# Kernel optimization log

Hardware: AMD Instinct MI355X
Metric: run time of the kernel (lower is better)

Reference implementation:

```python
import jax, jax.numpy as jnp
import numpy as np

P = 16                     # patch size
D = 192                    # embed dim (forced by SAT d_model=192)
NHEAD = 3                  # ViT-Tiny heads
SAT_H, SAT_DK, SAT_DV = 8, 32, 32
N_SLICE = 10
PER_LI = jnp.linspace(0.1, 1.0, N_SLICE)
LN_EPS = 1e-5


def layernorm(z, g, b):
    m = z.mean(-1, keepdims=True)
    v = ((z - m) ** 2).mean(-1, keepdims=True)
    return (z - m) * jax.lax.rsqrt(v + LN_EPS) * g + b


def setup_inputs() -> dict:
    key = jax.random.key(0)
    ks = jax.random.split(key, 32)
    B, IMG, DEPTH, MLP = 128, 224, 12, 4 * D
    S = (IMG // P) ** 2 + 1  # 197 tokens
    n = lambda k, sh: jax.random.normal(k, sh, jnp.float32) * 0.02
    z = lambda sh: jnp.zeros(sh, jnp.float32)
    o = lambda sh: jnp.ones(sh, jnp.float32)
    return {
        "x": jax.random.uniform(ks[0], (B, 3, IMG, IMG), jnp.float32),
        "x_g_norm": jax.random.uniform(ks[1], (B, 1, 56, 56), jnp.float32),
        "patch_w": n(ks[2], (D, 3, P, P)), "patch_b": z((D,)),
        "cls_token": n(ks[3], (1, 1, D)), "pos_embed": n(ks[4], (1, S, D)),
        "eleva_embed": n(ks[5], (1, D)),
        "sat_wq": n(ks[6], (D, SAT_H * SAT_DK)), "sat_bq": z((SAT_H * SAT_DK,)),
        "sat_wk": n(ks[7], (D, SAT_H * SAT_DK)), "sat_bk": z((SAT_H * SAT_DK,)),
        "sat_wv": n(ks[8], (D, SAT_H * SAT_DV)), "sat_bv": z((SAT_H * SAT_DV,)),
        "sat_wo": n(ks[9], (SAT_H * SAT_DV, D)), "sat_bo": z((D,)),
        "ln1_g": o((DEPTH, D)), "ln1_b": z((DEPTH, D)),
        "qkv_w": n(ks[10], (DEPTH, D, 3 * D)), "qkv_b": z((DEPTH, 3 * D)),
        "proj_w": n(ks[11], (DEPTH, D, D)), "proj_b": z((DEPTH, D)),
        "ln2_g": o((DEPTH, D)), "ln2_b": z((DEPTH, D)),
        "fc1_w": n(ks[12], (DEPTH, D, MLP)), "fc1_b": z((DEPTH, MLP)),
        "fc2_w": n(ks[13], (DEPTH, MLP, D)), "fc2_b": z((DEPTH, D)),
        "norm_g": o((D,)), "norm_b": z((D,)),
    }


def _forward(x, x_g_norm, patch_w, patch_b, cls_token, pos_embed, eleva_embed,
             sat_wq, sat_bq, sat_wk, sat_bk, sat_wv, sat_bv, sat_wo, sat_bo,
             ln1_g, ln1_b, qkv_w, qkv_b, proj_w, proj_b, ln2_g, ln2_b,
             fc1_w, fc1_b, fc2_w, fc2_b, norm_g, norm_b):
    B = x.shape[0]
    # --- patch embed: Conv2d(3, D, kernel=P, stride=P) -> [B, N, D] ---
    feat = jax.lax.conv_general_dilated(
        x, patch_w, (P, P), 'VALID', dimension_numbers=('NCHW', 'OIHW', 'NCHW'))
    feat = feat + patch_b[None, :, None, None]
    tokens = feat.reshape(B, D, -1).transpose(0, 2, 1)          # [B, 196, D]
    tok = jnp.concatenate([jnp.broadcast_to(cls_token, (B, 1, D)), tokens], axis=1)
    tok = tok + pos_embed                                        # [B, S, D]
    S = tok.shape[1]
    # --- elevation weight per sample (vectorized bisect + linear interp) ---
    means = x_g_norm.mean(axis=(1, 2, 3))                        # [B]
    idx = jnp.clip(jnp.searchsorted(PER_LI, means, side='left'), 0, N_SLICE - 1)
    per_hi = PER_LI[idx]
    per_lo = jnp.where(idx == 0, 0.0, PER_LI[jnp.maximum(idx - 1, 0)])
    idx_f = idx.astype(jnp.float32)
    idx_inter = idx_f - (per_hi - means) / (per_hi - per_lo)
    w = jnp.where(idx == N_SLICE - 1, idx_f, idx_inter) / N_SLICE  # [B]
    # --- SAT fusion: per (batch, token) a 2-element attention over (token, ele) ---
    ele = jnp.broadcast_to(eleva_embed[0] * w[:, None, None], tok.shape)  # [B,S,D]
    at_in = jnp.stack([tok, ele], axis=2)                        # [B, S, 2, D]
    q = (at_in @ sat_wq + sat_bq).reshape(B, S, 2, SAT_H, SAT_DK)
    k = (at_in @ sat_wk + sat_bk).reshape(B, S, 2, SAT_H, SAT_DK)
    v = (at_in @ sat_wv + sat_bv).reshape(B, S, 2, SAT_H, SAT_DV)
    att = jnp.einsum('bsqhd,bskhd->bshqk', q, k) * (1.0 / np.sqrt(SAT_DK))
    att = jax.nn.softmax(att, axis=-1)
    sat_o = jnp.einsum('bshqk,bskhd->bsqhd', att, v).reshape(B, S, 2, SAT_H * SAT_DV)
    sat_o = sat_o @ sat_wo + sat_bo                              # [B, S, 2, D]
    h = sat_o[..., 0, :] + sat_o[..., 1, :]                      # [B, S, D]
    # --- ViT blocks via scan over stacked layer params ---
    hd = D // NHEAD

    def block(z, p):
        l1g, l1b, qw, qb, pw, pb, l2g, l2b, f1w, f1b, f2w, f2b = p
        y = layernorm(z, l1g, l1b)
        qkv = y @ qw + qb                                        # [B, S, 3D]
        q_, k_, v_ = jnp.split(qkv, 3, axis=-1)
        q_ = q_.reshape(B, S, NHEAD, hd)
        k_ = k_.reshape(B, S, NHEAD, hd)
        v_ = v_.reshape(B, S, NHEAD, hd)
        a = jnp.einsum('bqhd,bkhd->bhqk', q_, k_) * (hd ** -0.5)
        a = jax.nn.softmax(a, axis=-1)
        o = jnp.einsum('bhqk,bkhd->bqhd', a, v_).reshape(B, S, D)
        z = z + o @ pw + pb
        y = layernorm(z, l2g, l2b)
        z = z + jax.nn.gelu(y @ f1w + f1b, approximate=False) @ f2w + f2b
        return z, None

    h, _ = jax.lax.scan(block, h, (ln1_g, ln1_b, qkv_w, qkv_b, proj_w, proj_b,
                                   ln2_g, ln2_b, fc1_w, fc1_b, fc2_w, fc2_b))
    h = layernorm(h, norm_g, norm_b)
    return h[:, 0]                                               # [B, D] cls token


def reference(x, x_g_norm, patch_w, patch_b, cls_token, pos_embed, eleva_embed,
              sat_wq, sat_bq, sat_wk, sat_bk, sat_wv, sat_bv, sat_wo, sat_bo,
              ln1_g, ln1_b, qkv_w, qkv_b, proj_w, proj_b, ln2_g, ln2_b,
              fc1_w, fc1_b, fc2_w, fc2_b, norm_g, norm_b):
    return _forward(x, x_g_norm, patch_w, patch_b, cls_token, pos_embed, eleva_embed,
                    sat_wq, sat_bq, sat_wk, sat_bk, sat_wv, sat_bv, sat_wo, sat_bo,
                    ln1_g, ln1_b, qkv_w, qkv_b, proj_w, proj_b, ln2_g, ln2_b,
                    fc1_w, fc1_b, fc2_w, fc2_b, norm_g, norm_b)
```

## Files before the change

kernel.cpp:

```cpp
#include <hip/hip_runtime.h>


#define BATCH 128
#define SEQ 197
#define BS_ROWS (BATCH * SEQ)
#define DMODEL 192
#define NPATCH 196
#define MROWS_PATCH (BATCH * NPATCH)
#define KPATCH 768
#define MLPDIM 768
#define DEPTH 12
#define SPAD 224

typedef float f32x4 __attribute__((ext_vector_type(4)));
typedef short s16x8 __attribute__((ext_vector_type(8)));

__device__ __forceinline__ float wredSum(float v) {
#pragma unroll
  for (int o = 32; o > 0; o >>= 1) v += __shfl_xor(v, o, 64);
  return v;
}

__device__ __forceinline__ unsigned short f2bf(float f) {
  union { float f; unsigned u; } v;
  v.f = f;
  unsigned r = v.u + 0x7FFFu + ((v.u >> 16) & 1u);
  return (unsigned short)(r >> 16);
}
__device__ __forceinline__ float bf2f(unsigned short u) {
  union { unsigned u; float f; } v;
  v.u = ((unsigned)u) << 16;
  return v.f;
}

__device__ __forceinline__ int swz(int col, int row) {
  int g8 = col >> 3;
  g8 = (g8 & ~7) | ((g8 & 7) ^ (row & 7));
  return (g8 << 3) | (col & 7);
}

__device__ __forceinline__ float gelu(float x) {
  const float ax = fabsf(x) * 0.70710678118654752f;
  const float t = 1.f / (1.f + 0.3275911f * ax);
  const float y =
      t * (0.254829592f +
           t * (-0.284496736f +
                t * (1.421413741f + t * (-1.453152027f + t * 1.061405429f))));
  const float erfc_ = y * __expf(-ax * ax);
  const float cdf = (x >= 0.f) ? (1.f - 0.5f * erfc_) : (0.5f * erfc_);
  return x * cdf;
}

__global__ __launch_bounds__(256) void eleva_w_kernel(const float* __restrict__ xg,
                                                      float* __restrict__ wout) {
  const int b = blockIdx.x;
  const float* p = xg + (size_t)b * 3136;
  float s = 0.f;
  for (int i = threadIdx.x; i < 3136; i += 256) s += p[i];
  __shared__ float partial[4];
  s = wredSum(s);
  if ((threadIdx.x & 63) == 0) partial[threadIdx.x >> 6] = s;
  __syncthreads();
  if (threadIdx.x == 0) {
    float m = (partial[0] + partial[1] + partial[2] + partial[3]) / 3136.f;
    int idx = 0;
#pragma unroll
    for (int i = 0; i < 10; i++) {
      float pv = 0.1f * (float)(i + 1);
      if (pv < m) idx = i + 1;
    }
    if (idx > 9) idx = 9;
    float wv;
    if (idx == 9) {
      wv = 9.f;
    } else {
      float hi = 0.1f * (float)(idx + 1);
      float lo = (idx == 0) ? 0.f : 0.1f * (float)idx;
      wv = (float)idx - (hi - m) / (hi - lo);
    }
    wout[b] = wv / 10.f;
  }
}

__global__ __launch_bounds__(256) void wtrans_kernel(const float* __restrict__ in,
                                                     unsigned short* __restrict__ out,
                                                     int R, int C) {
  const int z = blockIdx.z;
  in += (size_t)z * R * C;
  out += (size_t)z * R * C;
  const int c0 = blockIdx.x * 32, r0 = blockIdx.y * 32;
  __shared__ float t[32][33];
  const int tr = threadIdx.x >> 3, tc = (threadIdx.x & 7) * 4;
  const float4 v = *(const float4*)(in + (size_t)(r0 + tr) * C + c0 + tc);
  t[tr][tc] = v.x; t[tr][tc + 1] = v.y; t[tr][tc + 2] = v.z; t[tr][tc + 3] = v.w;
  __syncthreads();
  ushort4 o;
  o.x = f2bf(t[tc + 0][tr]);
  o.y = f2bf(t[tc + 1][tr]);
  o.z = f2bf(t[tc + 2][tr]);
  o.w = f2bf(t[tc + 3][tr]);
  const int brow = c0 + tr;
  *(ushort4*)(out + (size_t)brow * R + swz(r0 + tc, brow)) = o;
}

__global__ __launch_bounds__(256) void convert_kernel(const float* __restrict__ in,
                                                      unsigned short* __restrict__ out, int n4,
                                                      int K) {
  const int i = blockIdx.x * 256 + threadIdx.x;
  if (i >= n4) return;
  const int flat = i * 4;
  const int row = flat / K, col = flat % K;
  const float4 v = *(const float4*)(in + flat);
  ushort4 o;
  o.x = f2bf(v.x); o.y = f2bf(v.y); o.z = f2bf(v.z); o.w = f2bf(v.w);
  *(ushort4*)(out + (size_t)row * K + swz(col, row)) = o;
}

__global__ __launch_bounds__(256) void im2col_kernel(const float* __restrict__ x,
                                                     unsigned short* __restrict__ col) {
  const int i = blockIdx.x * 256 + threadIdx.x;
  if (i >= MROWS_PATCH * KPATCH / 8) return;
  const int k = (i % 96) * 8, row = i / 96;
  const int b = row / NPATCH, p = row % NPATCH;
  const int py = p / 14, px = p % 14;
  const int c = k >> 8, r = (k >> 4) & 15, cc = k & 15;
  const float* src = x + (((size_t)b * 3 + c) * 224 + (py * 16 + r)) * 224 + (px * 16 + cc);
  const float4 v0 = *(const float4*)src;
  const float4 v1 = *(const float4*)(src + 4);
  s16x8 o;
  o[0] = (short)f2bf(v0.x); o[1] = (short)f2bf(v0.y);
  o[2] = (short)f2bf(v0.z); o[3] = (short)f2bf(v0.w);
  o[4] = (short)f2bf(v1.x); o[5] = (short)f2bf(v1.y);
  o[6] = (short)f2bf(v1.z); o[7] = (short)f2bf(v1.w);
  *(s16x8*)(col + (size_t)row * KPATCH + swz(k, row)) = o;
}

__global__ __launch_bounds__(256) void cls_kernel(const float* __restrict__ cls,
                                                  const float* __restrict__ pos,
                                                  float* __restrict__ H,
                                                  unsigned short* __restrict__ Hbf) {
  const int i = blockIdx.x * 256 + threadIdx.x;
  if (i >= BATCH * DMODEL) return;
  const int b = i / DMODEL, d = i % DMODEL;
  const float v = cls[d] + pos[d];
  const int row = b * SEQ;
  H[(size_t)row * DMODEL + d] = v;
  Hbf[(size_t)row * DMODEL + swz(d, row)] = f2bf(v);
}

__global__ __launch_bounds__(256) void ele_proj_kernel(
    const float* __restrict__ ele_emb, const float* __restrict__ wq, const float* __restrict__ bq,
    const float* __restrict__ wk, const float* __restrict__ bk,
    const float* __restrict__ wv, const float* __restrict__ bv,
    const float* __restrict__ wvec, float* __restrict__ eq, float* __restrict__ ek,
    float* __restrict__ ev, float* __restrict__ satb) {
  const int b = blockIdx.x, t = threadIdx.x;
  if (b == 0) {
    satb[t] = bq[t];
    satb[256 + t] = bk[t];
    satb[512 + t] = bv[t];
  }
  __shared__ float es[DMODEL];
  if (t < DMODEL) es[t] = ele_emb[t] * wvec[b];
  __syncthreads();
  float aq = bq[t], ak = bk[t], av = bv[t];
  for (int d = 0; d < DMODEL; d++) {
    const float e = es[d];
    aq += e * wq[d * 256 + t];
    ak += e * wk[d * 256 + t];
    av += e * wv[d * 256 + t];
  }
  eq[b * 256 + t] = aq;
  ek[b * 256 + t] = ak;
  ev[b * 256 + t] = av;
}

__global__ __launch_bounds__(256) void sat_mix_kernel(
    const unsigned short* __restrict__ qkv768, const float* __restrict__ eq,
    const float* __restrict__ ek, const float* __restrict__ ev,
    unsigned short* __restrict__ o256) {
  const int gid = blockIdx.x * 256 + threadIdx.x;
  const int tok = gid >> 3, h = gid & 7;
  if (tok >= BS_ROWS) return;
  const int b = tok / SEQ;
  const unsigned short* qp = qkv768 + (size_t)tok * 768 + h * 32;
  s16x8 qv[4], kv[4];
#pragma unroll
  for (int i0 = 0; i0 < 4; i0++) {
    qv[i0] = *(const s16x8*)(qp + i0 * 8);
    kv[i0] = *(const s16x8*)(qp + 256 + i0 * 8);
  }
  float eqa[32], eka[32];
  {
    const float4* eqp = (const float4*)(eq + b * 256 + h * 32);
    const float4* ekp = (const float4*)(ek + b * 256 + h * 32);
#pragma unroll
    for (int i0 = 0; i0 < 8; i0++) {
      const float4 a = eqp[i0], c = ekp[i0];
      eqa[i0 * 4] = a.x; eqa[i0 * 4 + 1] = a.y; eqa[i0 * 4 + 2] = a.z; eqa[i0 * 4 + 3] = a.w;
      eka[i0 * 4] = c.x; eka[i0 * 4 + 1] = c.y; eka[i0 * 4 + 2] = c.z; eka[i0 * 4 + 3] = c.w;
    }
  }
  float s00 = 0.f, s01 = 0.f, s10 = 0.f, s11 = 0.f;
#pragma unroll
  for (int d = 0; d < 32; d++) {
    const float q_ = bf2f((unsigned short)qv[d >> 3][d & 7]);
    const float k_ = bf2f((unsigned short)kv[d >> 3][d & 7]);
    s00 += q_ * k_;
    s01 += q_ * eka[d];
    s10 += eqa[d] * k_;
    s11 += eqa[d] * eka[d];
  }
  const float sc = 0.17677669529663687f;
  s00 *= sc; s01 *= sc; s10 *= sc; s11 *= sc;
  const float m0 = fmaxf(s00, s01), m1 = fmaxf(s10, s11);
  const float e00 = __expf(s00 - m0), e01 = __expf(s01 - m0);
  const float e10 = __expf(s10 - m1), e11 = __expf(s11 - m1);
  const float w0 = e00 / (e00 + e01) + e10 / (e10 + e11);
  const float w1 = e01 / (e00 + e01) + e11 / (e10 + e11);
  unsigned short* op = o256 + (size_t)tok * 256;
  const float4* evp = (const float4*)(ev + b * 256 + h * 32);
#pragma unroll
  for (int i0 = 0; i0 < 4; i0++) {
    const s16x8 vv = *(const s16x8*)(qp + 512 + i0 * 8);
    const float4 e0 = evp[i0 * 2], e1 = evp[i0 * 2 + 1];
    float ev8[8] = {e0.x, e0.y, e0.z, e0.w, e1.x, e1.y, e1.z, e1.w};
    s16x8 o;
#pragma unroll
    for (int e = 0; e < 8; e++)
      o[e] = (short)f2bf(w0 * bf2f((unsigned short)vv[e]) + w1 * ev8[e]);
    *(s16x8*)(op + swz(h * 32 + i0 * 8, tok)) = o;
  }
}

template <int EPI, bool SWZO, int BN, int BM>
__global__ __launch_bounds__(256, 4)
void gemm_mfma(const unsigned short* __restrict__ A,
               const unsigned short* __restrict__ Bt,
               const float* __restrict__ bias,
               const float* __restrict__ res,
               void* __restrict__ Cout,
               unsigned short* __restrict__ aux_hbf,
               const float* __restrict__ aux_pos,
               const float* __restrict__ lng,
               const float* __restrict__ lnb,
               int M, int N, int K) {
  constexpr int NJ = 3;
  constexpr int MI = (BM == 128) ? 4 : 2;
  constexpr bool LNF = (EPI == 5 || EPI == 6);
  constexpr int LNROWS = LNF ? BM : 1;
  __shared__ unsigned short As[BM * 64];
  __shared__ unsigned short Bs[BN * 64];
  __shared__ float2 lnbuf[4][LNROWS];
  const int tid = threadIdx.x, lane = tid & 63, w = tid >> 6;
  const int n0 = blockIdx.x * BN;
  const int m0 = blockIdx.y * BM;
  const int c = lane & 15, g = lane >> 4;
  const int wm = (BM == 128) ? (w >> 1) * 64 : 0;
  const int wn = (BM == 128) ? (w & 1) * 96 / 2 : w * 48;
  f32x4 acc[MI][NJ] = {};

  const int ar = (lane >> 3);
  const int acol = (lane & 7) * 8;

  for (int k0 = 0; k0 < K; k0 += 64) {
#pragma unroll
    for (int it = 0; it < BM / 32; it++) {
      const int r = w * (BM / 4) + it * 8 + ar;
      const unsigned short* gp = A + (size_t)(m0 + r) * K + k0 + acol;
      __builtin_amdgcn_global_load_lds(
          (const __attribute__((address_space(1))) unsigned int*)gp,
          (__attribute__((address_space(3))) unsigned int*)(As + (w * (BM / 4) + it * 8) * 64),
          16, 0, 0);
    }
#pragma unroll
    for (int it = 0; it < BN / 32; it++) {
      const int r = w * (BN / 4) + it * 8 + ar;
      const unsigned short* gp = Bt + (size_t)(n0 + r) * K + k0 + acol;
      __builtin_amdgcn_global_load_lds(
          (const __attribute__((address_space(1))) unsigned int*)gp,
          (__attribute__((address_space(3))) unsigned int*)(Bs + (w * (BN / 4) + it * 8) * 64),
          16, 0, 0);
    }
    __syncthreads();
#pragma unroll
    for (int kk = 0; kk < 2; kk++) {
      const int sw = (((kk * 4 + g) ^ (c & 7))) << 3;
      s16x8 af[MI], bfr[NJ];
#pragma unroll
      for (int i = 0; i < MI; i++)
        af[i] = *(const s16x8*)&As[(wm + i * 16 + c) * 64 + sw];
#pragma unroll
      for (int j = 0; j < NJ; j++)
        bfr[j] = *(const s16x8*)&Bs[(wn + j * 16 + c) * 64 + sw];
#pragma unroll
      for (int i = 0; i < MI; i++)
#pragma unroll
        for (int j = 0; j < NJ; j++)
          acc[i][j] = __builtin_amdgcn_mfma_f32_16x16x32_bf16(af[i], bfr[j], acc[i][j], 0, 0, 0);
    }
    __syncthreads();
  }

  const int ncol0 = n0 + wn + c;
  float bv[NJ];
#pragma unroll
  for (int j = 0; j < NJ; j++) bv[j] = bias[ncol0 + j * 16] * (EPI == 6 ? 2.f : 1.f);

  if constexpr (LNF) {
#pragma unroll
    for (int i = 0; i < MI; i++) {
#pragma unroll
      for (int r_ = 0; r_ < 4; r_++) {
        const int lr = wm + i * 16 + g * 4 + r_;
        const int mrow = m0 + lr;
        float s1 = 0.f, s2 = 0.f;
#pragma unroll
        for (int j = 0; j < NJ; j++) {
          float v = acc[i][j][r_] + bv[j];
          if (EPI == 5) v += res[(size_t)mrow * DMODEL + ncol0 + j * 16];
          acc[i][j][r_] = v;
          ((float*)Cout)[(size_t)mrow * DMODEL + ncol0 + j * 16] = v;
          s1 += v;
          s2 += v * v;
        }
#pragma unroll
        for (int o = 1; o <= 8; o <<= 1) {
          s1 += __shfl_xor(s1, o, 64);
          s2 += __shfl_xor(s2, o, 64);
        }
        if (c == 0) lnbuf[w][lr] = make_float2(s1, s2);
      }
    }
    __syncthreads();
    float lg[NJ], lb[NJ];
#pragma unroll
    for (int j = 0; j < NJ; j++) { lg[j] = lng[ncol0 + j * 16]; lb[j] = lnb[ncol0 + j * 16]; }
#pragma unroll
    for (int i = 0; i < MI; i++) {
#pragma unroll
      for (int r_ = 0; r_ < 4; r_++) {
        const int lr = wm + i * 16 + g * 4 + r_;
        const int mrow = m0 + lr;
        const float2 a0 = lnbuf[0][lr], a1 = lnbuf[1][lr];
        const float2 a2 = lnbuf[2][lr], a3 = lnbuf[3][lr];
        const float mean = (a0.x + a1.x + a2.x + a3.x) * (1.f / 192.f);
        const float var = (a0.y + a1.y + a2.y + a3.y) * (1.f / 192.f) - mean * mean;
        const float inv = rsqrtf(var + 1e-5f);
#pragma unroll
        for (int j = 0; j < NJ; j++) {
          const int col = ncol0 + j * 16;
          const float yn = (acc[i][j][r_] - mean) * inv * lg[j] + lb[j];
          aux_hbf[(size_t)mrow * DMODEL + swz(col, mrow)] = f2bf(yn);
        }
      }
    }
  } else {
#pragma unroll
    for (int i = 0; i < MI; i++) {
#pragma unroll
      for (int r_ = 0; r_ < 4; r_++) {
        const int mrow = m0 + wm + i * 16 + g * 4 + r_;
        if (EPI == 4) {
          const int bb = mrow / 196;
          const int p = mrow - bb * 196;
          const int drow = mrow + bb + 1;
#pragma unroll
          for (int j = 0; j < NJ; j++) {
            const int col = ncol0 + j * 16;
            const float v = acc[i][j][r_] + bv[j] + aux_pos[(size_t)(p + 1) * DMODEL + col];
            ((float*)Cout)[(size_t)drow * DMODEL + col] = v;
            aux_hbf[(size_t)drow * DMODEL + swz(col, drow)] = f2bf(v);
          }
        } else {
#pragma unroll
          for (int j = 0; j < NJ; j++) {
            float v = acc[i][j][r_] + bv[j];
            const int col = ncol0 + j * 16;
            const size_t rowoff = (size_t)mrow * N;
            if (EPI == 0) {
              ((unsigned short*)Cout)[rowoff + (SWZO ? swz(col, mrow) : col)] = f2bf(v);
            } else {
              ((unsigned short*)Cout)[rowoff + (SWZO ? swz(col, mrow) : col)] = f2bf(gelu(v));
            }
          }
        }
      }
    }
  }
}

__global__ __launch_bounds__(256) void final_ln_kernel(const float* __restrict__ H,
                                                       const float* __restrict__ g,
                                                       const float* __restrict__ bta,
                                                       float* __restrict__ out) {
  const int w = threadIdx.x >> 6, lane = threadIdx.x & 63;
  const int bi = blockIdx.x * 4 + w;
  if (bi >= BATCH) return;
  const float* x = H + (size_t)bi * SEQ * DMODEL;
  const float x0 = x[lane], x1 = x[lane + 64], x2 = x[lane + 128];
  const float m = wredSum(x0 + x1 + x2) * (1.f / 192.f);
  const float d0 = x0 - m, d1 = x1 - m, d2 = x2 - m;
  const float v = wredSum(d0 * d0 + d1 * d1 + d2 * d2) * (1.f / 192.f);
  const float inv = rsqrtf(v + 1e-5f);
  float* y = out + (size_t)bi * DMODEL;
  y[lane] = d0 * inv * g[lane] + bta[lane];
  y[lane + 64] = d1 * inv * g[lane + 64] + bta[lane + 64];
  y[lane + 128] = d2 * inv * g[lane + 128] + bta[lane + 128];
}

__global__ __launch_bounds__(256) void vtrans_kernel(const unsigned short* __restrict__ qkv,
                                                     unsigned short* __restrict__ vt) {
  const int bid = blockIdx.x;
  const int sc = bid & 3, bh = bid >> 2;
  const int b = bh / 3, h = bh % 3;
  const int s0 = sc * 64;
  __shared__ unsigned short t[64][72];
  const int tid = threadIdx.x;
  for (int e = tid; e < 64 * 64; e += 256) {
    const int sp = e >> 6, d = e & 63;
    const int s = s0 + sp;
    t[sp][d] = (s < SEQ) ? qkv[((size_t)(b * SEQ + s)) * 576 + 384 + h * 64 + d] : (unsigned short)0;
  }
  __syncthreads();
  for (int e = tid; e < 64 * 64; e += 256) {
    const int d = e >> 6, sp = e & 63;
    const int s = s0 + sp;
    if (s < SPAD) vt[((size_t)bh * 64 + d) * SPAD + s] = t[sp][d];
  }
}

__global__ __launch_bounds__(64) void attn_mfma_kernel(const unsigned short* __restrict__ qkv,
                                                       const unsigned short* __restrict__ vt,
                                                       unsigned short* __restrict__ out) {
  const int bid = blockIdx.x;
  const int bh = bid / 13, qt = bid % 13;
  const int b = bh / 3, h = bh % 3;
  const int row0 = b * SEQ;
  const int q0 = qt * 16;
  const int lane = threadIdx.x;
  const int c = lane & 15, g = lane >> 4;

  __shared__ __attribute__((aligned(16))) unsigned short P[16][232];

  const int qr = row0 + min(q0 + c, SEQ - 1);
  const unsigned short* qp = qkv + (size_t)qr * 576 + h * 64 + g * 8;
  const s16x8 qlo = *(const s16x8*)qp;
  const s16x8 qhi = *(const s16x8*)(qp + 32);

  f32x4 acc[13];
#pragma unroll
  for (int t = 0; t < 13; t++) {
    const int kr = row0 + min(t * 16 + c, SEQ - 1);
    const unsigned short* kp = qkv + (size_t)kr * 576 + 192 + h * 64 + g * 8;
    const s16x8 klo = *(const s16x8*)kp;
    const s16x8 khi = *(const s16x8*)(kp + 32);
    f32x4 z = {0.f, 0.f, 0.f, 0.f};
    z = __builtin_amdgcn_mfma_f32_16x16x32_bf16(qlo, klo, z, 0, 0, 0);
    acc[t] = __builtin_amdgcn_mfma_f32_16x16x32_bf16(qhi, khi, z, 0, 0, 0);
  }

  const bool m12 = (c >= 5);
#pragma unroll
  for (int r = 0; r < 4; r++) {
    float mx = -INFINITY;
#pragma unroll
    for (int t = 0; t < 13; t++) {
      const float v = (t == 12 && m12) ? -INFINITY : acc[t][r];
      mx = fmaxf(mx, v);
    }
#pragma unroll
    for (int o = 1; o <= 8; o <<= 1) mx = fmaxf(mx, __shfl_xor(mx, o, 64));
    const float ms = mx * 0.125f;
    float sum = 0.f;
#pragma unroll
    for (int t = 0; t < 13; t++) {
      const float e = (t == 12 && m12) ? 0.f : __expf(acc[t][r] * 0.125f - ms);
      acc[t][r] = e;
      sum += e;
    }
#pragma unroll
    for (int o = 1; o <= 8; o <<= 1) sum += __shfl_xor(sum, o, 64);
    const float inv = 1.f / sum;
#pragma unroll
    for (int t = 0; t < 13; t++) P[g * 4 + r][t * 16 + c] = f2bf(acc[t][r] * inv);
  }
  {
    unsigned short z4[4] = {0, 0, 0, 0};
    *(uint2*)&P[c][208 + g * 4] = *(uint2*)z4;
  }
  __builtin_amdgcn_s_waitcnt(0);

  f32x4 oacc[4];
#pragma unroll
  for (int dt = 0; dt < 4; dt++) oacc[dt] = (f32x4){0.f, 0.f, 0.f, 0.f};
  const unsigned short* vbase = vt + (size_t)bh * 64 * SPAD;
#pragma unroll
  for (int ch = 0; ch < 7; ch++) {
    const s16x8 pa = *(const s16x8*)&P[c][ch * 32 + g * 8];
#pragma unroll
    for (int dt = 0; dt < 4; dt++) {
      const s16x8 vb = *(const s16x8*)(vbase + (size_t)(dt * 16 + c) * SPAD + ch * 32 + g * 8);
      oacc[dt] = __builtin_amdgcn_mfma_f32_16x16x32_bf16(pa, vb, oacc[dt], 0, 0, 0);
    }
  }

#pragma unroll
  for (int dt = 0; dt < 4; dt++) {
#pragma unroll
    for (int r = 0; r < 4; r++) {
      const int q = q0 + g * 4 + r;
      if (q < SEQ) {
        const int trow = row0 + q;
        out[(size_t)trow * DMODEL + swz(h * 64 + dt * 16 + c, trow)] = f2bf(oacc[dt][r]);
      }
    }
  }
}

extern "C" void kernel_launch(void* const* d_in, const int* in_sizes, int n_in,
                              void* d_out, int out_size, void* d_ws, size_t ws_size,
                              hipStream_t stream) {
  const float* x       = (const float*)d_in[0];
  const float* xg      = (const float*)d_in[1];
  const float* patch_w = (const float*)d_in[2];
  const float* patch_b = (const float*)d_in[3];
  const float* cls_tok = (const float*)d_in[4];
  const float* pos_emb = (const float*)d_in[5];
  const float* ele_emb = (const float*)d_in[6];
  const float* sat_wq  = (const float*)d_in[7];
  const float* sat_bq  = (const float*)d_in[8];
  const float* sat_wk  = (const float*)d_in[9];
  const float* sat_bk  = (const float*)d_in[10];
  const float* sat_wv  = (const float*)d_in[11];
  const float* sat_bv  = (const float*)d_in[12];
  const float* sat_wo  = (const float*)d_in[13];
  const float* sat_bo  = (const float*)d_in[14];
  const float* ln1_g   = (const float*)d_in[15];
  const float* ln1_b   = (const float*)d_in[16];
  const float* qkv_w   = (const float*)d_in[17];
  const float* qkv_b   = (const float*)d_in[18];
  const float* proj_w  = (const float*)d_in[19];
  const float* proj_b  = (const float*)d_in[20];
  const float* ln2_g   = (const float*)d_in[21];
  const float* ln2_b   = (const float*)d_in[22];
  const float* fc1_w   = (const float*)d_in[23];
  const float* fc1_b   = (const float*)d_in[24];
  const float* fc2_w   = (const float*)d_in[25];
  const float* fc2_b   = (const float*)d_in[26];
  const float* norm_g  = (const float*)d_in[27];
  const float* norm_b  = (const float*)d_in[28];
  float* out = (float*)d_out;
  float* ws = (float*)d_ws;

  float* W_ELE = ws;
  float* EQ = ws + 256;
  float* EK = EQ + 32768;
  float* EV = EK + 32768;
  float* H = ws + 98560;
  unsigned short* Hbf   = (unsigned short*)(ws + 4940032);
  unsigned short* Ybf   = (unsigned short*)(ws + 7360768);
  unsigned short* QKVbf = (unsigned short*)(ws + 9781504);
  unsigned short* MLPbf = (unsigned short*)(ws + 17043712);
  unsigned short* VTB   = (unsigned short*)(ws + 26726656);
  unsigned short* WTS   = (unsigned short*)(ws + 29479168);
  float* SATB = ws + 32305408;
  unsigned short* ATTNbf = (unsigned short*)(ws + 32306176);

  unsigned short* qkv_wt   = WTS;
  unsigned short* proj_wt  = WTS + 1327104;
  unsigned short* fc1_wt   = WTS + 1769472;
  unsigned short* fc2_wt   = WTS + 3538944;
  unsigned short* patch_bf = WTS + 5308416;
  unsigned short* satqkv_t = WTS + 5455872;
  unsigned short* sato_t   = WTS + 5603328;

  unsigned short* COLbf   = MLPbf;
  unsigned short* SATQKV  = MLPbf;
  unsigned short* O256bf  = QKVbf;

  wtrans_kernel<<<dim3(18, 6, 12), 256, 0, stream>>>(qkv_w, qkv_wt, 192, 576);
  wtrans_kernel<<<dim3(6, 6, 12), 256, 0, stream>>>(proj_w, proj_wt, 192, 192);
  wtrans_kernel<<<dim3(24, 6, 12), 256, 0, stream>>>(fc1_w, fc1_wt, 192, 768);
  wtrans_kernel<<<dim3(6, 24, 12), 256, 0, stream>>>(fc2_w, fc2_wt, 768, 192);
  wtrans_kernel<<<dim3(8, 6, 1), 256, 0, stream>>>(sat_wq, satqkv_t, 192, 256);
  wtrans_kernel<<<dim3(8, 6, 1), 256, 0, stream>>>(sat_wk, satqkv_t + 49152, 192, 256);
  wtrans_kernel<<<dim3(8, 6, 1), 256, 0, stream>>>(sat_wv, satqkv_t + 98304, 192, 256);
  wtrans_kernel<<<dim3(6, 8, 1), 256, 0, stream>>>(sat_wo, sato_t, 256, 192);
  convert_kernel<<<144, 256, 0, stream>>>(patch_w, patch_bf, 36864, KPATCH);

  eleva_w_kernel<<<BATCH, 256, 0, stream>>>(xg, W_ELE);

  im2col_kernel<<<(MROWS_PATCH * KPATCH / 8) / 256, 256, 0, stream>>>(x, COLbf);
  gemm_mfma<4, false, 96, 128><<<dim3(2, 196), 256, 0, stream>>>(
      COLbf, patch_bf, patch_b, nullptr, H, Hbf, pos_emb, nullptr, nullptr,
      MROWS_PATCH, DMODEL, KPATCH);
  cls_kernel<<<(BATCH * DMODEL) / 256, 256, 0, stream>>>(cls_tok, pos_emb, H, Hbf);

  ele_proj_kernel<<<BATCH, 256, 0, stream>>>(ele_emb, sat_wq, sat_bq, sat_wk, sat_bk,
                                             sat_wv, sat_bv, W_ELE, EQ, EK, EV, SATB);
  gemm_mfma<0, false, 96, 128><<<dim3(8, 197), 256, 0, stream>>>(
      Hbf, satqkv_t, SATB, nullptr, SATQKV, nullptr, nullptr, nullptr, nullptr,
      BS_ROWS, 768, DMODEL);
  sat_mix_kernel<<<BS_ROWS / 32, 256, 0, stream>>>(SATQKV, EQ, EK, EV, O256bf);
  gemm_mfma<6, false, 192, 32><<<dim3(1, 788), 256, 0, stream>>>(
      O256bf, sato_t, sat_bo, nullptr, H, Ybf, nullptr, ln1_g, ln1_b,
      BS_ROWS, DMODEL, 256);

  for (int l = 0; l < DEPTH; l++) {
    gemm_mfma<0, false, 96, 128><<<dim3(6, 197), 256, 0, stream>>>(
        Ybf, qkv_wt + (size_t)l * 110592, qkv_b + l * 576, nullptr, QKVbf, nullptr, nullptr,
        nullptr, nullptr, BS_ROWS, 576, DMODEL);
    vtrans_kernel<<<BATCH * 3 * 4, 256, 0, stream>>>(QKVbf, VTB);
    attn_mfma_kernel<<<BATCH * 3 * 13, 64, 0, stream>>>(QKVbf, VTB, ATTNbf);
    gemm_mfma<5, false, 192, 32><<<dim3(1, 788), 256, 0, stream>>>(
        ATTNbf, proj_wt + (size_t)l * 36864, proj_b + l * DMODEL, H, H, Ybf, nullptr,
        ln2_g + l * DMODEL, ln2_b + l * DMODEL, BS_ROWS, DMODEL, DMODEL);
    gemm_mfma<1, true, 96, 128><<<dim3(8, 197), 256, 0, stream>>>(
        Ybf, fc1_wt + (size_t)l * 147456, fc1_b + l * MLPDIM, nullptr, MLPbf, nullptr, nullptr,
        nullptr, nullptr, BS_ROWS, MLPDIM, DMODEL);
    const float* nlg = (l < DEPTH - 1) ? (ln1_g + (l + 1) * DMODEL) : norm_g;
    const float* nlb = (l < DEPTH - 1) ? (ln1_b + (l + 1) * DMODEL) : norm_b;
    gemm_mfma<5, false, 192, 32><<<dim3(1, 788), 256, 0, stream>>>(
        MLPbf, fc2_wt + (size_t)l * 147456, fc2_b + l * DMODEL, H, H, Ybf, nullptr,
        nlg, nlb, BS_ROWS, DMODEL, MLPDIM);
  }

  final_ln_kernel<<<BATCH / 4, 256, 0, stream>>>(H, norm_g, norm_b, out);
}
```

Baseline: 1.759 ms.

## Fuse V transpose into QKV GEMM epilogue and remap tile order for XCD locality

The QKV GEMM gains a new epilogue that writes the V columns straight into the transposed, padded VT buffer, which removes the separate vtrans kernel from every layer. The pad region is zeroed once by a memset. Separately, the BM=128 GEMMs now use a 1D grid, with block ids remapped so that groups of 8 consecutive blocks take different M tiles. This is meant to improve cache locality across the XCDs and rounds the grid up to a multiple of 8 with early exit. The risk is that the transposed epilogue makes scattered 2-byte strided stores.

```diff
diff --git a/kernel.cpp b/kernel.cpp
--- a/kernel.cpp
+++ b/kernel.cpp
@@ -244,17 +244,28 @@
                const float* __restrict__ aux_pos,
                const float* __restrict__ lng,
                const float* __restrict__ lnb,
-               int M, int N, int K) {
+               int M, int N, int K, int nx) {
   constexpr int NJ = 3;
   constexpr int MI = (BM == 128) ? 4 : 2;
   constexpr bool LNF = (EPI == 5 || EPI == 6);
   constexpr int LNROWS = LNF ? BM : 1;
+  int mt, nt;
+  if (BM == 128) {
+    const int bid = blockIdx.x;
+    const int e = bid & 7, i = bid >> 3;
+    nt = i % nx;
+    mt = e + 8 * (i / nx);
+    if (mt * BM >= M) return;
+  } else {
+    mt = blockIdx.y;
+    nt = blockIdx.x;
+  }
   __shared__ unsigned short As[BM * 64];
   __shared__ unsigned short Bs[BN * 64];
   __shared__ float2 lnbuf[4][LNROWS];
   const int tid = threadIdx.x, lane = tid & 63, w = tid >> 6;
-  const int n0 = blockIdx.x * BN;
-  const int m0 = blockIdx.y * BM;
+  const int n0 = nt * BN;
+  const int m0 = mt * BM;
   const int c = lane & 15, g = lane >> 4;
   const int wm = (BM == 128) ? (w >> 1) * 64 : 0;
   const int wn = (BM == 128) ? (w & 1) * 96 / 2 : w * 48;
@@ -355,6 +366,22 @@
         }
       }
     }
+  } else if (EPI == 7 && n0 >= 384) {
+#pragma unroll
+    for (int i = 0; i < MI; i++) {
+#pragma unroll
+      for (int r_ = 0; r_ < 4; r_++) {
+        const int mrow = m0 + wm + i * 16 + g * 4 + r_;
+        const int b = mrow / SEQ;
+        const int s = mrow - b * SEQ;
+#pragma unroll
+        for (int j = 0; j < NJ; j++) {
+          const int vcol = ncol0 + j * 16 - 384;
+          const int h = vcol >> 6, d = vcol & 63;
+          aux_hbf[((size_t)((b * 3 + h) * 64 + d)) * SPAD + s] = f2bf(acc[i][j][r_] + bv[j]);
+        }
+      }
+    }
   } else {
 #pragma unroll
     for (int i = 0; i < MI; i++) {
@@ -378,10 +405,10 @@
             float v = acc[i][j][r_] + bv[j];
             const int col = ncol0 + j * 16;
             const size_t rowoff = (size_t)mrow * N;
-            if (EPI == 0) {
+            if (EPI == 1) {
+              ((unsigned short*)Cout)[rowoff + (SWZO ? swz(col, mrow) : col)] = f2bf(gelu(v));
+            } else {
               ((unsigned short*)Cout)[rowoff + (SWZO ? swz(col, mrow) : col)] = f2bf(v);
-            } else {
-              ((unsigned short*)Cout)[rowoff + (SWZO ? swz(col, mrow) : col)] = f2bf(gelu(v));
             }
           }
         }
@@ -407,27 +434,6 @@
   y[lane] = d0 * inv * g[lane] + bta[lane];
   y[lane + 64] = d1 * inv * g[lane + 64] + bta[lane + 64];
   y[lane + 128] = d2 * inv * g[lane + 128] + bta[lane + 128];
-}
-
-__global__ __launch_bounds__(256) void vtrans_kernel(const unsigned short* __restrict__ qkv,
-                                                     unsigned short* __restrict__ vt) {
-  const int bid = blockIdx.x;
-  const int sc = bid & 3, bh = bid >> 2;
-  const int b = bh / 3, h = bh % 3;
-  const int s0 = sc * 64;
-  __shared__ unsigned short t[64][72];
-  const int tid = threadIdx.x;
-  for (int e = tid; e < 64 * 64; e += 256) {
-    const int sp = e >> 6, d = e & 63;
-    const int s = s0 + sp;
-    t[sp][d] = (s < SEQ) ? qkv[((size_t)(b * SEQ + s)) * 576 + 384 + h * 64 + d] : (unsigned short)0;
-  }
-  __syncthreads();
-  for (int e = tid; e < 64 * 64; e += 256) {
-    const int d = e >> 6, sp = e & 63;
-    const int s = s0 + sp;
-    if (s < SPAD) vt[((size_t)bh * 64 + d) * SPAD + s] = t[sp][d];
-  }
 }
 
 __global__ __launch_bounds__(64) void attn_mfma_kernel(const unsigned short* __restrict__ qkv,
@@ -579,6 +585,8 @@
   unsigned short* SATQKV  = MLPbf;
   unsigned short* O256bf  = QKVbf;
 
+  hipMemsetAsync(VTB, 0, (size_t)BATCH * 3 * 64 * SPAD * 2, stream);
+
   wtrans_kernel<<<dim3(18, 6, 12), 256, 0, stream>>>(qkv_w, qkv_wt, 192, 576);
   wtrans_kernel<<<dim3(6, 6, 12), 256, 0, stream>>>(proj_w, proj_wt, 192, 192);
   wtrans_kernel<<<dim3(24, 6, 12), 256, 0, stream>>>(fc1_w, fc1_wt, 192, 768);
@@ -592,38 +600,37 @@
   eleva_w_kernel<<<BATCH, 256, 0, stream>>>(xg, W_ELE);
 
   im2col_kernel<<<(MROWS_PATCH * KPATCH / 8) / 256, 256, 0, stream>>>(x, COLbf);
-  gemm_mfma<4, false, 96, 128><<<dim3(2, 196), 256, 0, stream>>>(
+  gemm_mfma<4, false, 96, 128><<<400, 256, 0, stream>>>(
       COLbf, patch_bf, patch_b, nullptr, H, Hbf, pos_emb, nullptr, nullptr,
-      MROWS_PATCH, DMODEL, KPATCH);
+      MROWS_PATCH, DMODEL, KPATCH, 2);
   cls_kernel<<<(BATCH * DMODEL) / 256, 256, 0, stream>>>(cls_tok, pos_emb, H, Hbf);
 
   ele_proj_kernel<<<BATCH, 256, 0, stream>>>(ele_emb, sat_wq, sat_bq, sat_wk, sat_bk,
                                              sat_wv, sat_bv, W_ELE, EQ, EK, EV, SATB);
-  gemm_mfma<0, false, 96, 128><<<dim3(8, 197), 256, 0, stream>>>(
+  gemm_mfma<0, false, 96, 128><<<1600, 256, 0, stream>>>(
       Hbf, satqkv_t, SATB, nullptr, SATQKV, nullptr, nullptr, nullptr, nullptr,
-      BS_ROWS, 768, DMODEL);
+      BS_ROWS, 768, DMODEL, 8);
   sat_mix_kernel<<<BS_ROWS / 32, 256, 0, stream>>>(SATQKV, EQ, EK, EV, O256bf);
   gemm_mfma<6, false, 192, 32><<<dim3(1, 788), 256, 0, stream>>>(
       O256bf, sato_t, sat_bo, nullptr, H, Ybf, nullptr, ln1_g, ln1_b,
-      BS_ROWS, DMODEL, 256);
+      BS_ROWS, DMODEL, 256, 1);
 
   for (int l = 0; l < DEPTH; l++) {
-    gemm_mfma<0, false, 96, 128><<<dim3(6, 197), 256, 0, stream>>>(
-        Ybf, qkv_wt + (size_t)l * 110592, qkv_b + l * 576, nullptr, QKVbf, nullptr, nullptr,
-        nullptr, nullptr, BS_ROWS, 576, DMODEL);
-    vtrans_kernel<<<BATCH * 3 * 4, 256, 0, stream>>>(QKVbf, VTB);
+    gemm_mfma<7, false, 96, 128><<<1200, 256, 0, stream>>>(
+        Ybf, qkv_wt + (size_t)l * 110592, qkv_b + l * 576, nullptr, QKVbf, VTB, nullptr,
+        nullptr, nullptr, BS_ROWS, 576, DMODEL, 6);
     attn_mfma_kernel<<<BATCH * 3 * 13, 64, 0, stream>>>(QKVbf, VTB, ATTNbf);
     gemm_mfma<5, false, 192, 32><<<dim3(1, 788), 256, 0, stream>>>(
         ATTNbf, proj_wt + (size_t)l * 36864, proj_b + l * DMODEL, H, H, Ybf, nullptr,
-        ln2_g + l * DMODEL, ln2_b + l * DMODEL, BS_ROWS, DMODEL, DMODEL);
-    gemm_mfma<1, true, 96, 128><<<dim3(8, 197), 256, 0, stream>>>(
+        ln2_g + l * DMODEL, ln2_b + l * DMODEL, BS_ROWS, DMODEL, DMODEL, 1);
+    gemm_mfma<1, true, 96, 128><<<1600, 256, 0, stream>>>(
         Ybf, fc1_wt + (size_t)l * 147456, fc1_b + l * MLPDIM, nullptr, MLPbf, nullptr, nullptr,
-        nullptr, nullptr, BS_ROWS, MLPDIM, DMODEL);
+        nullptr, nullptr, BS_ROWS, MLPDIM, DMODEL, 8);
     const float* nlg = (l < DEPTH - 1) ? (ln1_g + (l + 1) * DMODEL) : norm_g;
     const float* nlb = (l < DEPTH - 1) ? (ln1_b + (l + 1) * DMODEL) : norm_b;
     gemm_mfma<5, false, 192, 32><<<dim3(1, 788), 256, 0, stream>>>(
         MLPbf, fc2_wt + (size_t)l * 147456, fc2_b + l * DMODEL, H, H, Ybf, nullptr,
-        nlg, nlb, BS_ROWS, DMODEL, MLPDIM);
+        nlg, nlb, BS_ROWS, DMODEL, MLPDIM, 1);
   }
 
   final_ln_kernel<<<BATCH / 4, 256, 0, stream>>>(H, norm_g, norm_b, out);
```

Result: faster. 1.724 ms (-2.0%).
